# Kernel optimization log

Measured on AMD Instinct MI355X. Metric: run time of the kernel, lower is better.

The kernel has to match this reference:

```python
import jax, jax.numpy as jnp
import numpy as np

ALPHA = 0.5
NEG_MASK = 1000000.0


def setup_inputs() -> dict:
    key = jax.random.key(0)
    k1, k2, k3, k4 = jax.random.split(key, 4)
    B, Dv, Nq, Ns, D = 64, 1024, 32, 1024, 128
    return {
        "q_single": jax.random.normal(k1, (B, Dv), dtype=jnp.float32),
        "d_single": jax.random.normal(k2, (B, Dv), dtype=jnp.float32),
        "q_multi": jax.random.normal(k3, (B, Nq, D), dtype=jnp.float32),
        "d_multi": jax.random.normal(k4, (B, Ns, D), dtype=jnp.float32),
    }


def _single_vector_loss(q_single, d_single):
    # scores: [B, B]
    scores = jnp.einsum('bd,cd->bc', q_single, d_single)
    # MatryoshkaCELoss iterates rows of scores; each row is CE'd against its
    # diagonal target and the per-row losses are summed (relative_importance=None -> ones).
    logp = jax.nn.log_softmax(scores, axis=-1)
    return -jnp.sum(jnp.diagonal(logp))


def _multi_vector_loss(q_multi, d_multi):
    B = q_multi.shape[0]
    # [B, B, Nq, Ns] late-interaction score tensor -> max over doc tokens, sum over query tokens
    sim = jnp.einsum('bnd,csd->bcns', q_multi, d_multi)
    scores = jnp.sum(jnp.max(sim, axis=3), axis=2)  # [B, B]
    pos_scores = jnp.diagonal(scores)
    neg_scores = jnp.max(scores - jnp.eye(B, dtype=scores.dtype) * NEG_MASK, axis=1)
    return jnp.mean(jax.nn.softplus(neg_scores - pos_scores))


def reference(q_single, d_single, q_multi, d_multi):
    sv = _single_vector_loss(q_single, d_single)
    mv = _multi_vector_loss(q_multi, d_multi)
    return ALPHA * sv + (1.0 - ALPHA) * mv
```

## Files before the change

### kernel.cpp

```cpp
#include <hip/hip_runtime.h>
#include <hip/hip_bf16.h>
#include <math.h>

#define BSZ 64
#define DV  1024
#define NQ  32
#define NS  1024
#define DD  128

#define ALPHA 0.5f

#define BG 4
#define SC 128
#define ROWB 272

typedef __attribute__((ext_vector_type(8))) short short8;
typedef __attribute__((ext_vector_type(4))) float floatx4;

__global__ void cvt_bf16_kernel(const float* __restrict__ qm, const float* __restrict__ dm,
                                unsigned short* __restrict__ qb, unsigned short* __restrict__ db) {
    const int QG = (BSZ * NQ * DD) / 4;
    const int DG = (BSZ * NS * DD) / 4;
    int idx = blockIdx.x * blockDim.x + threadIdx.x;
    int stride = gridDim.x * blockDim.x;
    for (int g = idx; g < QG + DG; g += stride) {
        float4 v;
        unsigned short* dst;
        if (g < QG) { v = ((const float4*)qm)[g]; dst = qb + g * 4; }
        else        { int h = g - QG; v = ((const float4*)dm)[h]; dst = db + (size_t)h * 4; }
        __hip_bfloat16 a = __float2bfloat16(v.x);
        __hip_bfloat16 b = __float2bfloat16(v.y);
        __hip_bfloat16 c = __float2bfloat16(v.z);
        __hip_bfloat16 d = __float2bfloat16(v.w);
        ushort4 u;
        u.x = *(unsigned short*)&a; u.y = *(unsigned short*)&b;
        u.z = *(unsigned short*)&c; u.w = *(unsigned short*)&d;
        *(ushort4*)dst = u;
    }
}

__global__ void single_loss_kernel(const float* __restrict__ q, const float* __restrict__ d,
                                   float* __restrict__ out) {
    int b = blockIdx.x;
    int t = threadIdx.x;
    int c = t >> 2, part = t & 3;
    const float4* qv = (const float4*)(q + b * DV);
    const float4* dv = (const float4*)(d + c * DV);
    float acc = 0.f;
    int k0 = part * 64;
#pragma unroll 8
    for (int k = k0; k < k0 + 64; ++k) {
        float4 a = qv[k], bb = dv[k];
        acc += a.x * bb.x + a.y * bb.y + a.z * bb.z + a.w * bb.w;
    }
    acc += __shfl_xor(acc, 1);
    acc += __shfl_xor(acc, 2);
    __shared__ float row[BSZ];
    if (part == 0) row[c] = acc;
    __syncthreads();
    if (t < BSZ) {
        float v = row[t];
        float m = v;
#pragma unroll
        for (int o = 1; o < 64; o <<= 1) m = fmaxf(m, __shfl_xor(m, o));
        float e = expf(v - m);
#pragma unroll
        for (int o = 1; o < 64; o <<= 1) e += __shfl_xor(e, o);
        float lse = m + logf(e);
        if (t == 0) atomicAdd(out, ALPHA * (lse - row[b]));
    }
}

__launch_bounds__(256, 2)
__global__ void multi_scores_kernel(const unsigned short* __restrict__ qb,
                                    const unsigned short* __restrict__ db,
                                    float* __restrict__ scores) {
    int bg = blockIdx.x;
    int c  = blockIdx.y;
    int t  = threadIdx.x;
    int w  = t >> 6;
    int l  = t & 63;
    int lane16 = l & 15;
    int quad   = (l >> 4) & 3;

    __shared__ __align__(16) unsigned char dch[SC * ROWB];
    __shared__ float smax[4][BG][NQ];

    short8 af[BG][2][4];
#pragma unroll
    for (int bi = 0; bi < BG; ++bi)
#pragma unroll
        for (int nt = 0; nt < 2; ++nt)
#pragma unroll
            for (int ks = 0; ks < 4; ++ks)
                af[bi][nt][ks] = *(const short8*)(qb +
                    ((size_t)((bg * BG + bi) * NQ + nt * 16 + lane16) * DD + ks * 32 + quad * 8));

    float mx[BG][2][4];
#pragma unroll
    for (int bi = 0; bi < BG; ++bi)
#pragma unroll
        for (int nt = 0; nt < 2; ++nt)
#pragma unroll
            for (int r = 0; r < 4; ++r) mx[bi][nt][r] = -1e30f;

    const unsigned short* dbase = db + (size_t)c * NS * DD;

    for (int sc = 0; sc < NS / SC; ++sc) {
        __syncthreads();
        {
            const uint4* src = (const uint4*)(dbase + (size_t)sc * SC * DD);
#pragma unroll
            for (int p = 0; p < 8; ++p) {
                int f = t + p * 256;
                int row = f >> 4, col = f & 15;
                *(uint4*)(dch + row * ROWB + col * 16) = src[f];
            }
        }
        __syncthreads();
#pragma unroll
        for (int sti = 0; sti < 2; ++sti) {
            int st = w + sti * 4;
            short8 bf[4];
#pragma unroll
            for (int ks = 0; ks < 4; ++ks)
                bf[ks] = *(const short8*)(dch + (st * 16 + lane16) * ROWB + ks * 64 + quad * 16);
            floatx4 acc[BG][2];
#pragma unroll
            for (int bi = 0; bi < BG; ++bi)
#pragma unroll
                for (int nt = 0; nt < 2; ++nt) acc[bi][nt] = (floatx4){0.f, 0.f, 0.f, 0.f};
#pragma unroll
            for (int ks = 0; ks < 4; ++ks)
#pragma unroll
                for (int bi = 0; bi < BG; ++bi)
#pragma unroll
                    for (int nt = 0; nt < 2; ++nt)
                        acc[bi][nt] = __builtin_amdgcn_mfma_f32_16x16x32_bf16(
                            af[bi][nt][ks], bf[ks], acc[bi][nt], 0, 0, 0);
#pragma unroll
            for (int bi = 0; bi < BG; ++bi)
#pragma unroll
                for (int nt = 0; nt < 2; ++nt)
#pragma unroll
                    for (int r = 0; r < 4; ++r)
                        mx[bi][nt][r] = fmaxf(mx[bi][nt][r], acc[bi][nt][r]);
        }
    }

#pragma unroll
    for (int bi = 0; bi < BG; ++bi)
#pragma unroll
        for (int nt = 0; nt < 2; ++nt)
#pragma unroll
            for (int r = 0; r < 4; ++r) {
                float v = mx[bi][nt][r];
                v = fmaxf(v, __shfl_xor(v, 1));
                v = fmaxf(v, __shfl_xor(v, 2));
                v = fmaxf(v, __shfl_xor(v, 4));
                v = fmaxf(v, __shfl_xor(v, 8));
                mx[bi][nt][r] = v;
            }
    __syncthreads();
    if (lane16 == 0) {
#pragma unroll
        for (int bi = 0; bi < BG; ++bi)
#pragma unroll
            for (int nt = 0; nt < 2; ++nt)
#pragma unroll
                for (int r = 0; r < 4; ++r)
                    smax[w][bi][nt * 16 + quad * 4 + r] = mx[bi][nt][r];
    }
    __syncthreads();
    if (t < BG * NQ) {
        int bi = t >> 5, n = t & 31;
        float v = fmaxf(fmaxf(smax[0][bi][n], smax[1][bi][n]),
                        fmaxf(smax[2][bi][n], smax[3][bi][n]));
#pragma unroll
        for (int o = 1; o < 32; o <<= 1) v += __shfl_xor(v, o);
        if (n == 0) scores[(bg * BG + bi) * BSZ + c] = v;
    }
}

__global__ void finish_kernel(const float* __restrict__ scores, float* __restrict__ out) {
    int t = threadIdx.x;
    float pos = scores[t * BSZ + t];
    float neg = -1e30f;
    for (int cc = 0; cc < BSZ; ++cc)
        if (cc != t) neg = fmaxf(neg, scores[t * BSZ + cc]);
    float x = neg - pos;
    float sp = fmaxf(x, 0.f) + log1pf(expf(-fabsf(x)));
#pragma unroll
    for (int o = 1; o < 64; o <<= 1) sp += __shfl_xor(sp, o);
    if (t == 0) atomicAdd(out, (1.0f - ALPHA) * sp * (1.0f / BSZ));
}

extern "C" void kernel_launch(void* const* d_in, const int* in_sizes, int n_in,
                              void* d_out, int out_size, void* d_ws, size_t ws_size,
                              hipStream_t stream) {
    const float* q_single = (const float*)d_in[0];
    const float* d_single = (const float*)d_in[1];
    const float* q_multi  = (const float*)d_in[2];
    const float* d_multi  = (const float*)d_in[3];
    float* out = (float*)d_out;

    unsigned short* qb = (unsigned short*)d_ws;
    unsigned short* db = (unsigned short*)((char*)d_ws + 524288);
    float* scores      = (float*)((char*)d_ws + 524288 + 16777216);

    hipMemsetAsync(d_out, 0, sizeof(float), stream);
    cvt_bf16_kernel<<<1024, 256, 0, stream>>>(q_multi, d_multi, qb, db);
    single_loss_kernel<<<BSZ, 256, 0, stream>>>(q_single, d_single, out);
    multi_scores_kernel<<<dim3(16, 64), 256, 0, stream>>>(qb, db, scores);
    finish_kernel<<<1, 64, 0, stream>>>(scores, out);
}
```

Baseline: 150.7 us.

## Merge prep kernels, drop memset, load doc tiles directly into registers

The bf16 conversion and single-vector loss now run as one launch, and the final loss is written directly, with no memset or atomics. The multi-vector kernel no longer stages document chunks through shared memory with barriers. Each wave instead loads its MFMA B fragments straight from global memory, double-buffered across 16 tiles. This removes launch overhead and LDS/sync cost, but relies on global/L2 bandwidth for the doc reads and raises register pressure.

```diff
diff --git a/kernel.cpp b/kernel.cpp
--- a/kernel.cpp
+++ b/kernel.cpp
@@ -9,65 +9,64 @@
 #define DD  128
 
 #define ALPHA 0.5f
-
 #define BG 4
-#define SC 128
-#define ROWB 272
+#define CVT_BLOCKS 2048
 
 typedef __attribute__((ext_vector_type(8))) short short8;
 typedef __attribute__((ext_vector_type(4))) float floatx4;
 
-__global__ void cvt_bf16_kernel(const float* __restrict__ qm, const float* __restrict__ dm,
-                                unsigned short* __restrict__ qb, unsigned short* __restrict__ db) {
-    const int QG = (BSZ * NQ * DD) / 4;
-    const int DG = (BSZ * NS * DD) / 4;
-    int idx = blockIdx.x * blockDim.x + threadIdx.x;
-    int stride = gridDim.x * blockDim.x;
-    for (int g = idx; g < QG + DG; g += stride) {
-        float4 v;
-        unsigned short* dst;
-        if (g < QG) { v = ((const float4*)qm)[g]; dst = qb + g * 4; }
-        else        { int h = g - QG; v = ((const float4*)dm)[h]; dst = db + (size_t)h * 4; }
-        __hip_bfloat16 a = __float2bfloat16(v.x);
-        __hip_bfloat16 b = __float2bfloat16(v.y);
-        __hip_bfloat16 c = __float2bfloat16(v.z);
-        __hip_bfloat16 d = __float2bfloat16(v.w);
-        ushort4 u;
-        u.x = *(unsigned short*)&a; u.y = *(unsigned short*)&b;
-        u.z = *(unsigned short*)&c; u.w = *(unsigned short*)&d;
-        *(ushort4*)dst = u;
-    }
-}
-
-__global__ void single_loss_kernel(const float* __restrict__ q, const float* __restrict__ d,
-                                   float* __restrict__ out) {
-    int b = blockIdx.x;
-    int t = threadIdx.x;
-    int c = t >> 2, part = t & 3;
-    const float4* qv = (const float4*)(q + b * DV);
-    const float4* dv = (const float4*)(d + c * DV);
-    float acc = 0.f;
-    int k0 = part * 64;
+__global__ void prep_kernel(const float* __restrict__ qm, const float* __restrict__ dm,
+                            const float* __restrict__ qs, const float* __restrict__ ds,
+                            unsigned short* __restrict__ qb, unsigned short* __restrict__ db,
+                            float* __restrict__ svrow) {
+    __shared__ float row[BSZ];
+    if (blockIdx.x < CVT_BLOCKS) {
+        const int QG = (BSZ * NQ * DD) / 4;
+        const int DG = (BSZ * NS * DD) / 4;
+        int idx = blockIdx.x * blockDim.x + threadIdx.x;
+        int stride = CVT_BLOCKS * blockDim.x;
+        for (int g = idx; g < QG + DG; g += stride) {
+            float4 v;
+            unsigned short* dst;
+            if (g < QG) { v = ((const float4*)qm)[g]; dst = qb + g * 4; }
+            else        { int h = g - QG; v = ((const float4*)dm)[h]; dst = db + (size_t)h * 4; }
+            __hip_bfloat16 a = __float2bfloat16(v.x);
+            __hip_bfloat16 b = __float2bfloat16(v.y);
+            __hip_bfloat16 c = __float2bfloat16(v.z);
+            __hip_bfloat16 d = __float2bfloat16(v.w);
+            ushort4 u;
+            u.x = *(unsigned short*)&a; u.y = *(unsigned short*)&b;
+            u.z = *(unsigned short*)&c; u.w = *(unsigned short*)&d;
+            *(ushort4*)dst = u;
+        }
+    } else {
+        int b = blockIdx.x - CVT_BLOCKS;
+        int t = threadIdx.x;
+        int c = t >> 2, part = t & 3;
+        const float4* qv = (const float4*)(qs + b * DV);
+        const float4* dv = (const float4*)(ds + c * DV);
+        float acc = 0.f;
+        int k0 = part * 64;
 #pragma unroll 8
-    for (int k = k0; k < k0 + 64; ++k) {
-        float4 a = qv[k], bb = dv[k];
-        acc += a.x * bb.x + a.y * bb.y + a.z * bb.z + a.w * bb.w;
-    }
-    acc += __shfl_xor(acc, 1);
-    acc += __shfl_xor(acc, 2);
-    __shared__ float row[BSZ];
-    if (part == 0) row[c] = acc;
-    __syncthreads();
-    if (t < BSZ) {
-        float v = row[t];
-        float m = v;
-#pragma unroll
-        for (int o = 1; o < 64; o <<= 1) m = fmaxf(m, __shfl_xor(m, o));
-        float e = expf(v - m);
-#pragma unroll
-        for (int o = 1; o < 64; o <<= 1) e += __shfl_xor(e, o);
-        float lse = m + logf(e);
-        if (t == 0) atomicAdd(out, ALPHA * (lse - row[b]));
+        for (int k = k0; k < k0 + 64; ++k) {
+            float4 a = qv[k], bb = dv[k];
+            acc += a.x * bb.x + a.y * bb.y + a.z * bb.z + a.w * bb.w;
+        }
+        acc += __shfl_xor(acc, 1);
+        acc += __shfl_xor(acc, 2);
+        if (part == 0) row[c] = acc;
+        __syncthreads();
+        if (t < BSZ) {
+            float v = row[t];
+            float m = v;
+#pragma unroll
+            for (int o = 1; o < 64; o <<= 1) m = fmaxf(m, __shfl_xor(m, o));
+            float e = expf(v - m);
+#pragma unroll
+            for (int o = 1; o < 64; o <<= 1) e += __shfl_xor(e, o);
+            float lse = m + logf(e);
+            if (t == 0) svrow[b] = lse - row[b];
+        }
     }
 }
 
@@ -83,7 +82,6 @@
     int lane16 = l & 15;
     int quad   = (l >> 4) & 3;
 
-    __shared__ __align__(16) unsigned char dch[SC * ROWB];
     __shared__ float smax[4][BG][NQ];
 
     short8 af[BG][2][4];
@@ -104,48 +102,49 @@
 #pragma unroll
             for (int r = 0; r < 4; ++r) mx[bi][nt][r] = -1e30f;
 
-    const unsigned short* dbase = db + (size_t)c * NS * DD;
-
-    for (int sc = 0; sc < NS / SC; ++sc) {
-        __syncthreads();
-        {
-            const uint4* src = (const uint4*)(dbase + (size_t)sc * SC * DD);
-#pragma unroll
-            for (int p = 0; p < 8; ++p) {
-                int f = t + p * 256;
-                int row = f >> 4, col = f & 15;
-                *(uint4*)(dch + row * ROWB + col * 16) = src[f];
-            }
-        }
-        __syncthreads();
-#pragma unroll
-        for (int sti = 0; sti < 2; ++sti) {
-            int st = w + sti * 4;
-            short8 bf[4];
-#pragma unroll
-            for (int ks = 0; ks < 4; ++ks)
-                bf[ks] = *(const short8*)(dch + (st * 16 + lane16) * ROWB + ks * 64 + quad * 16);
-            floatx4 acc[BG][2];
+    const unsigned short* dptr = db + (size_t)c * NS * DD + (w * 16 + lane16) * DD + quad * 8;
+
+    short8 bfA[4], bfB[4];
+#pragma unroll
+    for (int ks = 0; ks < 4; ++ks) bfA[ks] = *(const short8*)(dptr + ks * 32);
+
+    auto tile_compute = [&](const short8* bf) {
+        floatx4 acc[BG][2];
+#pragma unroll
+        for (int bi = 0; bi < BG; ++bi)
+#pragma unroll
+            for (int nt = 0; nt < 2; ++nt) acc[bi][nt] = (floatx4){0.f, 0.f, 0.f, 0.f};
+#pragma unroll
+        for (int ks = 0; ks < 4; ++ks)
 #pragma unroll
             for (int bi = 0; bi < BG; ++bi)
 #pragma unroll
-                for (int nt = 0; nt < 2; ++nt) acc[bi][nt] = (floatx4){0.f, 0.f, 0.f, 0.f};
-#pragma unroll
-            for (int ks = 0; ks < 4; ++ks)
-#pragma unroll
-                for (int bi = 0; bi < BG; ++bi)
-#pragma unroll
-                    for (int nt = 0; nt < 2; ++nt)
-                        acc[bi][nt] = __builtin_amdgcn_mfma_f32_16x16x32_bf16(
-                            af[bi][nt][ks], bf[ks], acc[bi][nt], 0, 0, 0);
-#pragma unroll
-            for (int bi = 0; bi < BG; ++bi)
-#pragma unroll
                 for (int nt = 0; nt < 2; ++nt)
-#pragma unroll
-                    for (int r = 0; r < 4; ++r)
-                        mx[bi][nt][r] = fmaxf(mx[bi][nt][r], acc[bi][nt][r]);
-        }
+                    acc[bi][nt] = __builtin_amdgcn_mfma_f32_16x16x32_bf16(
+                        af[bi][nt][ks], bf[ks], acc[bi][nt], 0, 0, 0);
+#pragma unroll
+        for (int bi = 0; bi < BG; ++bi)
+#pragma unroll
+            for (int nt = 0; nt < 2; ++nt)
+#pragma unroll
+                for (int r = 0; r < 4; ++r)
+                    mx[bi][nt][r] = fmaxf(mx[bi][nt][r], acc[bi][nt][r]);
+    };
+
+#pragma unroll
+    for (int i = 0; i < 16; i += 2) {
+        if (i + 1 < 16) {
+            const unsigned short* p = dptr + (size_t)(i + 1) * 64 * DD;
+#pragma unroll
+            for (int ks = 0; ks < 4; ++ks) bfB[ks] = *(const short8*)(p + ks * 32);
+        }
+        tile_compute(bfA);
+        if (i + 2 < 16) {
+            const unsigned short* p = dptr + (size_t)(i + 2) * 64 * DD;
+#pragma unroll
+            for (int ks = 0; ks < 4; ++ks) bfA[ks] = *(const short8*)(p + ks * 32);
+        }
+        tile_compute(bfB);
     }
 
 #pragma unroll
@@ -161,7 +160,6 @@
                 v = fmaxf(v, __shfl_xor(v, 8));
                 mx[bi][nt][r] = v;
             }
-    __syncthreads();
     if (lane16 == 0) {
 #pragma unroll
         for (int bi = 0; bi < BG; ++bi)
@@ -182,7 +180,8 @@
     }
 }
 
-__global__ void finish_kernel(const float* __restrict__ scores, float* __restrict__ out) {
+__global__ void finish_kernel(const float* __restrict__ scores, const float* __restrict__ svrow,
+                              float* __restrict__ out) {
     int t = threadIdx.x;
     float pos = scores[t * BSZ + t];
     float neg = -1e30f;
@@ -190,9 +189,13 @@
         if (cc != t) neg = fmaxf(neg, scores[t * BSZ + cc]);
     float x = neg - pos;
     float sp = fmaxf(x, 0.f) + log1pf(expf(-fabsf(x)));
-#pragma unroll
-    for (int o = 1; o < 64; o <<= 1) sp += __shfl_xor(sp, o);
-    if (t == 0) atomicAdd(out, (1.0f - ALPHA) * sp * (1.0f / BSZ));
+    float sv = svrow[t];
+#pragma unroll
+    for (int o = 1; o < 64; o <<= 1) {
+        sp += __shfl_xor(sp, o);
+        sv += __shfl_xor(sv, o);
+    }
+    if (t == 0) out[0] = ALPHA * sv + (1.0f - ALPHA) * (sp * (1.0f / BSZ));
 }
 
 extern "C" void kernel_launch(void* const* d_in, const int* in_sizes, int n_in,
@@ -207,10 +210,10 @@
     unsigned short* qb = (unsigned short*)d_ws;
     unsigned short* db = (unsigned short*)((char*)d_ws + 524288);
     float* scores      = (float*)((char*)d_ws + 524288 + 16777216);
-
-    hipMemsetAsync(d_out, 0, sizeof(float), stream);
-    cvt_bf16_kernel<<<1024, 256, 0, stream>>>(q_multi, d_multi, qb, db);
-    single_loss_kernel<<<BSZ, 256, 0, stream>>>(q_single, d_single, out);
+    float* svrow       = (float*)((char*)d_ws + 524288 + 16777216 + 16384);
+
+    prep_kernel<<<CVT_BLOCKS + BSZ, 256, 0, stream>>>(q_multi, d_multi, q_single, d_single,
+                                                      qb, db, svrow);
     multi_scores_kernel<<<dim3(16, 64), 256, 0, stream>>>(qb, db, scores);
-    finish_kernel<<<1, 64, 0, stream>>>(scores, out);
-}
+    finish_kernel<<<1, 64, 0, stream>>>(scores, svrow, out);
+}
```

New measurement: 186.1 us. 1.23x slower.
